# Kernel tuning notes

Hardware: AMD Instinct MI355X
Metric: run time of the kernel (lower is better)

The kernel has to match this reference:

```python
import jax, jax.numpy as jnp
import numpy as np

N, E, G = 40000, 640000, 64
D, H, O = 128, 128, 10
EPS = 1e-5


def _lin(k, fan_in, shape):
    b = 1.0 / np.sqrt(fan_in)
    return jax.random.uniform(k, shape, jnp.float32, -b, b)


def setup_inputs() -> dict:
    key = jax.random.key(0)
    ks = jax.random.split(key, 12)
    x = jax.random.normal(ks[0], (N, D), jnp.float32)
    edge_index = jax.random.randint(ks[1], (2, E), 0, N)
    batch = jnp.sort(jax.random.randint(ks[2], (N,), 0, G))
    return {
        "x": x,
        "edge_index": edge_index,
        "batch": batch,
        "num_graphs": G,
        "W_gcn": _lin(ks[3], D, (D, H)),
        "b_gcn": jnp.zeros((H,), jnp.float32),
        "gamma": jnp.ones((H,), jnp.float32),
        "beta": jnp.zeros((H,), jnp.float32),
        "W1": _lin(ks[4], 3 * H, (3 * H, H)),
        "b1": _lin(ks[5], 3 * H, (H,)),
        "W2": _lin(ks[6], H, (H, H // 2)),
        "b2": _lin(ks[7], H, (H // 2,)),
        "W3": _lin(ks[8], H // 2, (H // 2, O)),
        "b3": _lin(ks[9], H // 2, (O,)),
    }


def reference(x, edge_index, batch, num_graphs, W_gcn, b_gcn, gamma, beta, W1, b1, W2, b2, W3, b3):
    n = x.shape[0]
    src, dst = edge_index[0], edge_index[1]
    # GCNConv: h = D^{-1/2} (A + I) D^{-1/2} (x W) + b  (self-loops, symmetric norm)
    h = x @ W_gcn                                   # [N, H]
    deg = jax.ops.segment_sum(jnp.ones((src.shape[0],), h.dtype), dst, num_segments=n) + 1.0
    dinv = jax.lax.rsqrt(deg)                       # [N]
    coef = dinv[src] * dinv[dst]                    # [E]
    msg = h[src] * coef[:, None]                    # [E, H] gather (memory bound)
    agg = jax.ops.segment_sum(msg, dst, num_segments=n)
    agg = agg + h * (dinv * dinv)[:, None] + b_gcn  # self-loop term + bias
    h = jax.nn.relu(agg)
    # LayerNorm over feature dim
    mu = jnp.mean(h, axis=-1, keepdims=True)
    var = jnp.mean(jnp.square(h - mu), axis=-1, keepdims=True)
    h = (h - mu) * jax.lax.rsqrt(var + EPS) * gamma + beta
    # global mean / add / max pools keyed by graph id
    counts = jax.ops.segment_sum(jnp.ones((n,), h.dtype), batch, num_segments=num_graphs)
    x_add = jax.ops.segment_sum(h, batch, num_segments=num_graphs)
    x_mean = x_add / jnp.maximum(counts, 1.0)[:, None]
    x_max = jax.ops.segment_max(h, batch, num_segments=num_graphs)
    x_max = jnp.where(counts[:, None] > 0, x_max, 0.0)
    g = jnp.concatenate([x_mean, x_add, x_max], axis=1)  # [G, 3H]
    # MLP head (dropout is identity at inference)
    g = jax.nn.relu(g @ W1 + b1)
    g = jax.nn.relu(g @ W2 + b2)
    return g @ W3 + b3
```

## Files before the change

### kernel.cpp

```cpp
#include <hip/hip_runtime.h>
#include <math.h>

#define EPS 1e-5f
#define FLT_BIG 3.402823466e38f

typedef __attribute__((ext_vector_type(8))) short bf16x8;
typedef __attribute__((ext_vector_type(4))) float f32x4;

__device__ __forceinline__ unsigned fflip(float f){
  int i = __float_as_int(f);
  return (unsigned)(i ^ ((i>>31) | 0x80000000));
}
__device__ __forceinline__ float funflip(unsigned u){
  int i = (u & 0x80000000u) ? (int)(u ^ 0x80000000u) : (int)(~u);
  return __int_as_float(i);
}
__device__ __forceinline__ unsigned f2bf(float f){
  unsigned u = __float_as_uint(f);
  return (u + 0x7FFFu + ((u>>16)&1u)) >> 16;
}
__device__ __forceinline__ float bf_lo(unsigned v){ return __uint_as_float(v<<16); }
__device__ __forceinline__ float bf_hi(unsigned v){ return __uint_as_float(v & 0xFFFF0000u); }

__device__ __forceinline__ int lbound(const int* __restrict__ a, int n, int key){
  int lo=0, hi=n;
  while(lo<hi){ int mid=(lo+hi)>>1; if(a[mid]<key) lo=mid+1; else hi=mid; }
  return lo;
}

__global__ __launch_bounds__(256) void k_init(
    int* __restrict__ cursor, int N,
    unsigned* __restrict__ psum, unsigned* __restrict__ pmaxu, int GP,
    const float* __restrict__ Wg, ushort* __restrict__ Wp){
  int i = blockIdx.x*blockDim.x + threadIdx.x;
  if(i<N) cursor[i] = 0;
  if(i<GP){ psum[i]=0u; pmaxu[i]=0u; }
  if(i<2048){
    int tile = i>>6, l = i&63;
    int kt = tile>>3, ct = tile&7;
    int q = l>>4, nn = l&15;
    ushort w8[8];
    #pragma unroll
    for(int j=0;j<8;j++)
      w8[j] = (ushort)f2bf(Wg[(kt*32 + q*8 + j)*128 + ct*16 + nn]);
    ushort* dst = Wp + (size_t)i*8;
    #pragma unroll
    for(int j=0;j<8;j++) dst[j] = w8[j];
  }
}

__global__ void k_scatter(const int* __restrict__ src, const int* __restrict__ dst, int E,
                          int* __restrict__ cursor, int* __restrict__ csr){
  int i = blockIdx.x*blockDim.x + threadIdx.x;
  int e = i<<2;
  if((E&3)==0){
    if(e<E){
      int4 s4 = *(const int4*)(src+e);
      int4 d4 = *(const int4*)(dst+e);
      int p;
      p = atomicAdd(&cursor[d4.x],1); if(p<64) csr[(d4.x<<6)+p] = s4.x;
      p = atomicAdd(&cursor[d4.y],1); if(p<64) csr[(d4.y<<6)+p] = s4.y;
      p = atomicAdd(&cursor[d4.z],1); if(p<64) csr[(d4.z<<6)+p] = s4.z;
      p = atomicAdd(&cursor[d4.w],1); if(p<64) csr[(d4.w<<6)+p] = s4.w;
    }
  } else {
    #pragma unroll
    for(int j=0;j<4;j++){
      int ee = e+j;
      if(ee<E){
        int s = src[ee], d = dst[ee];
        int p = atomicAdd(&cursor[d],1);
        if(p<64) csr[(d<<6)+p] = s;
      }
    }
  }
}

__global__ __launch_bounds__(256) void k_scale(
    const float4* __restrict__ x4, int nq, const int* __restrict__ cursor,
    uint2* __restrict__ xs2){
  int i = blockIdx.x*blockDim.x + threadIdx.x;
  if(i>=nq) return;
  int node = i>>5;
  int deg = cursor[node]; if(deg>64) deg=64;
  float dinv = rsqrtf((float)deg + 1.0f);
  float4 v = x4[i];
  uint2 o;
  o.x = (f2bf(v.y*dinv)<<16) | f2bf(v.x*dinv);
  o.y = (f2bf(v.w*dinv)<<16) | f2bf(v.z*dinv);
  xs2[i] = o;
}

__global__ void k_agg(const uint4* __restrict__ xs4, const int* __restrict__ cursor,
                      const int* __restrict__ csr, int n, uint4* __restrict__ zb4){
  int w = (blockIdx.x*blockDim.x + threadIdx.x)>>6;
  if(w>=n) return;
  int lane = threadIdx.x & 63;
  int grp = lane>>4, li = lane&15;
  int deg = cursor[w]; if(deg>64) deg=64;
  int k0 = w<<6, k1 = k0+deg;
  float dd = rsqrtf((float)deg + 1.0f);
  float a0=0.f,a1=0.f,a2=0.f,a3=0.f,a4=0.f,a5=0.f,a6=0.f,a7=0.f;
  if(grp==0){
    uint4 sv = xs4[(w<<4)+li];
    a0=bf_lo(sv.x); a1=bf_hi(sv.x); a2=bf_lo(sv.y); a3=bf_hi(sv.y);
    a4=bf_lo(sv.z); a5=bf_hi(sv.z); a6=bf_lo(sv.w); a7=bf_hi(sv.w);
  }
  for(int kb=k0; kb<k1; kb+=16){
    int base = kb + (grp<<2);
    int4 s4 = *(const int4*)(csr + base);
    if(base   < k1){ uint4 v = xs4[(s4.x<<4)+li];
      a0+=bf_lo(v.x); a1+=bf_hi(v.x); a2+=bf_lo(v.y); a3+=bf_hi(v.y);
      a4+=bf_lo(v.z); a5+=bf_hi(v.z); a6+=bf_lo(v.w); a7+=bf_hi(v.w); }
    if(base+1 < k1){ uint4 v = xs4[(s4.y<<4)+li];
      a0+=bf_lo(v.x); a1+=bf_hi(v.x); a2+=bf_lo(v.y); a3+=bf_hi(v.y);
      a4+=bf_lo(v.z); a5+=bf_hi(v.z); a6+=bf_lo(v.w); a7+=bf_hi(v.w); }
    if(base+2 < k1){ uint4 v = xs4[(s4.z<<4)+li];
      a0+=bf_lo(v.x); a1+=bf_hi(v.x); a2+=bf_lo(v.y); a3+=bf_hi(v.y);
      a4+=bf_lo(v.z); a5+=bf_hi(v.z); a6+=bf_lo(v.w); a7+=bf_hi(v.w); }
    if(base+3 < k1){ uint4 v = xs4[(s4.w<<4)+li];
      a0+=bf_lo(v.x); a1+=bf_hi(v.x); a2+=bf_lo(v.y); a3+=bf_hi(v.y);
      a4+=bf_lo(v.z); a5+=bf_hi(v.z); a6+=bf_lo(v.w); a7+=bf_hi(v.w); }
  }
  a0 += __shfl_xor(a0,16,64); a1 += __shfl_xor(a1,16,64);
  a2 += __shfl_xor(a2,16,64); a3 += __shfl_xor(a3,16,64);
  a4 += __shfl_xor(a4,16,64); a5 += __shfl_xor(a5,16,64);
  a6 += __shfl_xor(a6,16,64); a7 += __shfl_xor(a7,16,64);
  a0 += __shfl_xor(a0,32,64); a1 += __shfl_xor(a1,32,64);
  a2 += __shfl_xor(a2,32,64); a3 += __shfl_xor(a3,32,64);
  a4 += __shfl_xor(a4,32,64); a5 += __shfl_xor(a5,32,64);
  a6 += __shfl_xor(a6,32,64); a7 += __shfl_xor(a7,32,64);
  if(grp==0){
    uint4 o;
    o.x = (f2bf(a1*dd)<<16) | f2bf(a0*dd);
    o.y = (f2bf(a3*dd)<<16) | f2bf(a2*dd);
    o.z = (f2bf(a5*dd)<<16) | f2bf(a4*dd);
    o.w = (f2bf(a7*dd)<<16) | f2bf(a6*dd);
    zb4[(w<<4)+li] = o;
  }
}

__global__ __launch_bounds__(256) void k_gemmln(
    const unsigned* __restrict__ zb, const ushort* __restrict__ Wp,
    const float* __restrict__ bgc, const float* __restrict__ gamma, const float* __restrict__ beta,
    const int* __restrict__ batch, int n,
    float* __restrict__ pool_sum, unsigned* __restrict__ pool_maxu){
  __shared__ unsigned ztu[64*68];
  int t = threadIdx.x, lane = t & 63, wv = t >> 6;
  int rowBase = blockIdx.x*64;
  {
    int row = t>>2, qo = (t&3)*16;
    unsigned* lp = ztu + row*68 + qo;
    if(rowBase+row < n){
      const uint4* gp = (const uint4*)(zb + (size_t)(rowBase+row)*64 + qo);
      #pragma unroll
      for(int i=0;i<4;i++) ((uint4*)lp)[i] = gp[i];
    }else{
      #pragma unroll
      for(int i=0;i<4;i++) ((uint4*)lp)[i] = make_uint4(0,0,0,0);
    }
  }
  __syncthreads();

  int q = lane>>4, nn = lane&15;
  int m = wv*16 + nn;
  bf16x8 afr[4];
  #pragma unroll
  for(int kt=0;kt<4;kt++)
    afr[kt] = *(const bf16x8*)((const char*)ztu + m*272 + kt*64 + q*16);

  f32x4 acc[8];
  #pragma unroll
  for(int ct=0;ct<8;ct++){
    f32x4 c = {0.f,0.f,0.f,0.f};
    #pragma unroll
    for(int kt=0;kt<4;kt++){
      bf16x8 bfr = *(const bf16x8*)(Wp + ((size_t)(kt*8+ct)*64 + lane)*8);
      c = __builtin_amdgcn_mfma_f32_16x16x32_bf16(afr[kt], bfr, c, 0, 0, 0);
    }
    acc[ct] = c;
  }
  float s[4]={0,0,0,0}, qq[4]={0,0,0,0};
  #pragma unroll
  for(int ct=0;ct<8;ct++){
    float bb = bgc[ct*16+nn];
    #pragma unroll
    for(int r=0;r<4;r++){
      float v = acc[ct][r] + bb;
      v = fmaxf(v, 0.f);
      acc[ct][r] = v;
      s[r] += v; qq[r] += v*v;
    }
  }
  #pragma unroll
  for(int d=1; d<16; d<<=1){
    #pragma unroll
    for(int r=0;r<4;r++){
      s[r]  += __shfl_xor(s[r],  d, 64);
      qq[r] += __shfl_xor(qq[r], d, 64);
    }
  }
  float mu[4], isd[4];
  #pragma unroll
  for(int r=0;r<4;r++){
    mu[r] = s[r]*(1.f/128.f);
    float var = qq[r]*(1.f/128.f) - mu[r]*mu[r];
    isd[r] = rsqrtf(var + EPS);
  }
  #pragma unroll
  for(int ct=0;ct<8;ct++){
    float gm = gamma[ct*16+nn], bt = beta[ct*16+nn];
    #pragma unroll
    for(int r=0;r<4;r++)
      acc[ct][r] = (acc[ct][r]-mu[r])*isd[r]*gm + bt;
  }
  int gbr[4];
  #pragma unroll
  for(int r=0;r<4;r++){
    int gr = rowBase + wv*16 + q*4 + r;
    gbr[r] = (gr < n) ? batch[gr] : -1;
  }
  int b0i = rowBase + wv*16; if(b0i >= n) b0i = n-1;
  int b15i = rowBase + wv*16 + 15; if(b15i >= n) b15i = n-1;
  int gmin = batch[b0i], gmax = batch[b15i];
  if(gmax < gmin) gmax = gmin;
  for(int g=gmin; g<=gmax; ++g){
    #pragma unroll
    for(int ct=0;ct<8;ct++){
      float ssum = 0.f, smax = -FLT_BIG;
      #pragma unroll
      for(int r=0;r<4;r++){
        if(gbr[r]==g){
          ssum += acc[ct][r];
          smax = fmaxf(smax, acc[ct][r]);
        }
      }
      ssum += __shfl_xor(ssum, 16, 64);
      ssum += __shfl_xor(ssum, 32, 64);
      float o1 = __shfl_xor(smax, 16, 64); smax = fmaxf(smax, o1);
      float o2 = __shfl_xor(smax, 32, 64); smax = fmaxf(smax, o2);
      if(q==0){
        if(ssum != 0.f)   atomicAdd(&pool_sum[g*128 + ct*16 + nn], ssum);
        if(smax > -FLT_BIG) atomicMax(&pool_maxu[g*128 + ct*16 + nn], fflip(smax));
      }
    }
  }
}

__global__ void k_head(const float* __restrict__ pool_sum, const unsigned* __restrict__ pool_maxu,
                       const int* __restrict__ batch, int n,
                       const float* __restrict__ W1, const float* __restrict__ b1,
                       const float* __restrict__ W2, const float* __restrict__ b2,
                       const float* __restrict__ W3, const float* __restrict__ b3,
                       float* __restrict__ out){
  int g = blockIdx.x, t = threadIdx.x;
  __shared__ float red[2][128];
  __shared__ float gl[384];
  __shared__ float h1[128];
  __shared__ float h2[64];
  __shared__ int cnt_s;
  if(t==0){
    int s = lbound(batch,n,g), e = lbound(batch,n,g+1);
    cnt_s = e - s;
  }
  __syncthreads();
  int cnt = cnt_s;
  if(t<128){
    float s = pool_sum[g*128+t];
    gl[128+t] = s;
    gl[t] = s / (float)((cnt>1)?cnt:1);
    float m = funflip(pool_maxu[g*128+t]);
    gl[256+t] = (cnt>0) ? m : 0.f;
  }
  __syncthreads();
  int j = t & 127, kh = t >> 7;
  float p=0.f;
  for(int k=kh*192; k<kh*192+192; k++) p += gl[k]*W1[k*128+j];
  red[kh][j]=p;
  __syncthreads();
  if(t<128){
    float v = red[0][t]+red[1][t]+b1[t];
    h1[t]=fmaxf(v,0.f);
  }
  __syncthreads();
  if(t<64){
    float a=b2[t];
    for(int k=0;k<128;k++) a += h1[k]*W2[k*64+t];
    h2[t]=fmaxf(a,0.f);
  }
  __syncthreads();
  if(t<10){
    float a=b3[t];
    for(int k=0;k<64;k++) a += h2[k]*W3[k*10+t];
    out[g*10+t]=a;
  }
}

extern "C" void kernel_launch(void* const* d_in, const int* in_sizes, int n_in,
                              void* d_out, int out_size, void* d_ws, size_t ws_size,
                              hipStream_t stream){
  const float* x     = (const float*)d_in[0];
  const int*   ei    = (const int*)d_in[1];
  const int*   batch = (const int*)d_in[2];
  const float* Wg    = (const float*)d_in[4];
  const float* bg    = (const float*)d_in[5];
  const float* gamma = (const float*)d_in[6];
  const float* beta  = (const float*)d_in[7];
  const float* W1    = (const float*)d_in[8];
  const float* b1    = (const float*)d_in[9];
  const float* W2    = (const float*)d_in[10];
  const float* b2    = (const float*)d_in[11];
  const float* W3    = (const float*)d_in[12];
  const float* b3    = (const float*)d_in[13];
  float* out = (float*)d_out;

  int N = in_sizes[0]/128;
  int E = in_sizes[1]/2;
  const int G = 64;
  const int* src = ei;
  const int* dst = ei + E;

  char* p = (char*)d_ws;
  auto alloc=[&](size_t bytes)->char*{ char* r=p; p += (bytes+255)&~(size_t)255; return r; };
  int*      cursor = (int*)     alloc((size_t)N*4);
  int*      csr    = (int*)     alloc((size_t)N*64*4);
  unsigned* zb     = (unsigned*)alloc((size_t)N*64*4);
  float*    psum   = (float*)   alloc((size_t)G*128*4);
  unsigned* pmaxu  = (unsigned*)alloc((size_t)G*128*4);
  unsigned* xs     = (unsigned*)alloc((size_t)N*64*4);
  ushort*   Wp     = (ushort*)  alloc(2048*8*2);

  int GP = G*128;
  int nq = N*32;
  int ib = (N+255)/256;
  k_init<<<ib,256,0,stream>>>(cursor,N,(unsigned*)psum,pmaxu,GP,Wg,Wp);
  int eb = (E/4 + 255)/256;
  k_scatter<<<eb,256,0,stream>>>(src,dst,E,cursor,csr);
  int sb = (nq+255)/256;
  k_scale<<<sb,256,0,stream>>>((const float4*)x,nq,cursor,(uint2*)xs);
  int ab = (int)(((size_t)N*64 + 255)/256);
  k_agg<<<ab,256,0,stream>>>((const uint4*)xs,cursor,csr,N,(uint4*)zb);
  k_gemmln<<<(N+63)/64,256,0,stream>>>(zb,Wp,bg,gamma,beta,batch,N,psum,pmaxu);
  k_head<<<G,256,0,stream>>>(psum,pmaxu,batch,N,W1,b1,W2,b2,W3,b3,out);
}
```

Baseline: 180.9 us.

## Fuse neighbor aggregation with GEMM/LayerNorm/pooling and precompute graph counts

```diff
diff --git a/kernel.cpp b/kernel.cpp
--- a/kernel.cpp
+++ b/kernel.cpp
@@ -31,10 +31,15 @@
 __global__ __launch_bounds__(256) void k_init(
     int* __restrict__ cursor, int N,
     unsigned* __restrict__ psum, unsigned* __restrict__ pmaxu, int GP,
-    const float* __restrict__ Wg, ushort* __restrict__ Wp){
+    const float* __restrict__ Wg, ushort* __restrict__ Wp,
+    const int* __restrict__ batch, int* __restrict__ gcnt, int G){
   int i = blockIdx.x*blockDim.x + threadIdx.x;
   if(i<N) cursor[i] = 0;
   if(i<GP){ psum[i]=0u; pmaxu[i]=0u; }
+  if(i<G){
+    int s = lbound(batch,N,i), e = lbound(batch,N,i+1);
+    gcnt[i] = e - s;
+  }
   if(i<2048){
     int tile = i>>6, l = i&63;
     int kt = tile>>3, ct = tile&7;
@@ -91,83 +96,74 @@
   xs2[i] = o;
 }
 
-__global__ void k_agg(const uint4* __restrict__ xs4, const int* __restrict__ cursor,
-                      const int* __restrict__ csr, int n, uint4* __restrict__ zb4){
-  int w = (blockIdx.x*blockDim.x + threadIdx.x)>>6;
-  if(w>=n) return;
-  int lane = threadIdx.x & 63;
+__global__ __launch_bounds__(256) void k_aggemm(
+    const uint4* __restrict__ xs4, const int* __restrict__ cursor,
+    const int* __restrict__ csr, int n,
+    const ushort* __restrict__ Wp,
+    const float* __restrict__ bgc, const float* __restrict__ gamma, const float* __restrict__ beta,
+    const int* __restrict__ batch,
+    float* __restrict__ pool_sum, unsigned* __restrict__ pool_maxu){
+  __shared__ unsigned ztu[16*68];
+  int t = threadIdx.x, lane = t & 63, wv = t >> 6;
   int grp = lane>>4, li = lane&15;
-  int deg = cursor[w]; if(deg>64) deg=64;
-  int k0 = w<<6, k1 = k0+deg;
-  float dd = rsqrtf((float)deg + 1.0f);
-  float a0=0.f,a1=0.f,a2=0.f,a3=0.f,a4=0.f,a5=0.f,a6=0.f,a7=0.f;
-  if(grp==0){
-    uint4 sv = xs4[(w<<4)+li];
-    a0=bf_lo(sv.x); a1=bf_hi(sv.x); a2=bf_lo(sv.y); a3=bf_hi(sv.y);
-    a4=bf_lo(sv.z); a5=bf_hi(sv.z); a6=bf_lo(sv.w); a7=bf_hi(sv.w);
-  }
-  for(int kb=k0; kb<k1; kb+=16){
-    int base = kb + (grp<<2);
-    int4 s4 = *(const int4*)(csr + base);
-    if(base   < k1){ uint4 v = xs4[(s4.x<<4)+li];
-      a0+=bf_lo(v.x); a1+=bf_hi(v.x); a2+=bf_lo(v.y); a3+=bf_hi(v.y);
-      a4+=bf_lo(v.z); a5+=bf_hi(v.z); a6+=bf_lo(v.w); a7+=bf_hi(v.w); }
-    if(base+1 < k1){ uint4 v = xs4[(s4.y<<4)+li];
-      a0+=bf_lo(v.x); a1+=bf_hi(v.x); a2+=bf_lo(v.y); a3+=bf_hi(v.y);
-      a4+=bf_lo(v.z); a5+=bf_hi(v.z); a6+=bf_lo(v.w); a7+=bf_hi(v.w); }
-    if(base+2 < k1){ uint4 v = xs4[(s4.z<<4)+li];
-      a0+=bf_lo(v.x); a1+=bf_hi(v.x); a2+=bf_lo(v.y); a3+=bf_hi(v.y);
-      a4+=bf_lo(v.z); a5+=bf_hi(v.z); a6+=bf_lo(v.w); a7+=bf_hi(v.w); }
-    if(base+3 < k1){ uint4 v = xs4[(s4.w<<4)+li];
-      a0+=bf_lo(v.x); a1+=bf_hi(v.x); a2+=bf_lo(v.y); a3+=bf_hi(v.y);
-      a4+=bf_lo(v.z); a5+=bf_hi(v.z); a6+=bf_lo(v.w); a7+=bf_hi(v.w); }
-  }
-  a0 += __shfl_xor(a0,16,64); a1 += __shfl_xor(a1,16,64);
-  a2 += __shfl_xor(a2,16,64); a3 += __shfl_xor(a3,16,64);
-  a4 += __shfl_xor(a4,16,64); a5 += __shfl_xor(a5,16,64);
-  a6 += __shfl_xor(a6,16,64); a7 += __shfl_xor(a7,16,64);
-  a0 += __shfl_xor(a0,32,64); a1 += __shfl_xor(a1,32,64);
-  a2 += __shfl_xor(a2,32,64); a3 += __shfl_xor(a3,32,64);
-  a4 += __shfl_xor(a4,32,64); a5 += __shfl_xor(a5,32,64);
-  a6 += __shfl_xor(a6,32,64); a7 += __shfl_xor(a7,32,64);
-  if(grp==0){
-    uint4 o;
-    o.x = (f2bf(a1*dd)<<16) | f2bf(a0*dd);
-    o.y = (f2bf(a3*dd)<<16) | f2bf(a2*dd);
-    o.z = (f2bf(a5*dd)<<16) | f2bf(a4*dd);
-    o.w = (f2bf(a7*dd)<<16) | f2bf(a6*dd);
-    zb4[(w<<4)+li] = o;
-  }
-}
-
-__global__ __launch_bounds__(256) void k_gemmln(
-    const unsigned* __restrict__ zb, const ushort* __restrict__ Wp,
-    const float* __restrict__ bgc, const float* __restrict__ gamma, const float* __restrict__ beta,
-    const int* __restrict__ batch, int n,
-    float* __restrict__ pool_sum, unsigned* __restrict__ pool_maxu){
-  __shared__ unsigned ztu[64*68];
-  int t = threadIdx.x, lane = t & 63, wv = t >> 6;
-  int rowBase = blockIdx.x*64;
-  {
-    int row = t>>2, qo = (t&3)*16;
-    unsigned* lp = ztu + row*68 + qo;
-    if(rowBase+row < n){
-      const uint4* gp = (const uint4*)(zb + (size_t)(rowBase+row)*64 + qo);
-      #pragma unroll
-      for(int i=0;i<4;i++) ((uint4*)lp)[i] = gp[i];
-    }else{
-      #pragma unroll
-      for(int i=0;i<4;i++) ((uint4*)lp)[i] = make_uint4(0,0,0,0);
-    }
-  }
-  __syncthreads();
+  int rowBase = blockIdx.x*16;
+
+  for(int j=0;j<4;j++){
+    int rl = wv*4 + j;
+    int node = rowBase + rl;
+    float a0=0.f,a1=0.f,a2=0.f,a3=0.f,a4=0.f,a5=0.f,a6=0.f,a7=0.f;
+    float dd = 1.f;
+    if(node < n){
+      int deg = cursor[node]; if(deg>64) deg=64;
+      dd = rsqrtf((float)deg + 1.0f);
+      int k0 = node<<6, k1 = k0+deg;
+      if(grp==0){
+        uint4 sv = xs4[(node<<4)+li];
+        a0=bf_lo(sv.x); a1=bf_hi(sv.x); a2=bf_lo(sv.y); a3=bf_hi(sv.y);
+        a4=bf_lo(sv.z); a5=bf_hi(sv.z); a6=bf_lo(sv.w); a7=bf_hi(sv.w);
+      }
+      for(int kb=k0; kb<k1; kb+=16){
+        int base = kb + (grp<<2);
+        int4 s4 = *(const int4*)(csr + base);
+        if(base   < k1){ uint4 v = xs4[(s4.x<<4)+li];
+          a0+=bf_lo(v.x); a1+=bf_hi(v.x); a2+=bf_lo(v.y); a3+=bf_hi(v.y);
+          a4+=bf_lo(v.z); a5+=bf_hi(v.z); a6+=bf_lo(v.w); a7+=bf_hi(v.w); }
+        if(base+1 < k1){ uint4 v = xs4[(s4.y<<4)+li];
+          a0+=bf_lo(v.x); a1+=bf_hi(v.x); a2+=bf_lo(v.y); a3+=bf_hi(v.y);
+          a4+=bf_lo(v.z); a5+=bf_hi(v.z); a6+=bf_lo(v.w); a7+=bf_hi(v.w); }
+        if(base+2 < k1){ uint4 v = xs4[(s4.z<<4)+li];
+          a0+=bf_lo(v.x); a1+=bf_hi(v.x); a2+=bf_lo(v.y); a3+=bf_hi(v.y);
+          a4+=bf_lo(v.z); a5+=bf_hi(v.z); a6+=bf_lo(v.w); a7+=bf_hi(v.w); }
+        if(base+3 < k1){ uint4 v = xs4[(s4.w<<4)+li];
+          a0+=bf_lo(v.x); a1+=bf_hi(v.x); a2+=bf_lo(v.y); a3+=bf_hi(v.y);
+          a4+=bf_lo(v.z); a5+=bf_hi(v.z); a6+=bf_lo(v.w); a7+=bf_hi(v.w); }
+      }
+    }
+    a0 += __shfl_xor(a0,16,64); a1 += __shfl_xor(a1,16,64);
+    a2 += __shfl_xor(a2,16,64); a3 += __shfl_xor(a3,16,64);
+    a4 += __shfl_xor(a4,16,64); a5 += __shfl_xor(a5,16,64);
+    a6 += __shfl_xor(a6,16,64); a7 += __shfl_xor(a7,16,64);
+    a0 += __shfl_xor(a0,32,64); a1 += __shfl_xor(a1,32,64);
+    a2 += __shfl_xor(a2,32,64); a3 += __shfl_xor(a3,32,64);
+    a4 += __shfl_xor(a4,32,64); a5 += __shfl_xor(a5,32,64);
+    a6 += __shfl_xor(a6,32,64); a7 += __shfl_xor(a7,32,64);
+    if(grp==0){
+      uint4 o;
+      o.x = (f2bf(a1*dd)<<16) | f2bf(a0*dd);
+      o.y = (f2bf(a3*dd)<<16) | f2bf(a2*dd);
+      o.z = (f2bf(a5*dd)<<16) | f2bf(a4*dd);
+      o.w = (f2bf(a7*dd)<<16) | f2bf(a6*dd);
+      ((uint4*)(ztu + rl*68))[li] = o;
+    }
+  }
+  __syncthreads();
+  if(wv != 0) return;
 
   int q = lane>>4, nn = lane&15;
-  int m = wv*16 + nn;
   bf16x8 afr[4];
   #pragma unroll
   for(int kt=0;kt<4;kt++)
-    afr[kt] = *(const bf16x8*)((const char*)ztu + m*272 + kt*64 + q*16);
+    afr[kt] = *(const bf16x8*)((const char*)ztu + nn*272 + kt*64 + q*16);
 
   f32x4 acc[8];
   #pragma unroll
@@ -217,11 +213,11 @@
   int gbr[4];
   #pragma unroll
   for(int r=0;r<4;r++){
-    int gr = rowBase + wv*16 + q*4 + r;
+    int gr = rowBase + q*4 + r;
     gbr[r] = (gr < n) ? batch[gr] : -1;
   }
-  int b0i = rowBase + wv*16; if(b0i >= n) b0i = n-1;
-  int b15i = rowBase + wv*16 + 15; if(b15i >= n) b15i = n-1;
+  int b0i = rowBase; if(b0i >= n) b0i = n-1;
+  int b15i = rowBase + 15; if(b15i >= n) b15i = n-1;
   int gmin = batch[b0i], gmax = batch[b15i];
   if(gmax < gmin) gmax = gmin;
   for(int g=gmin; g<=gmax; ++g){
@@ -240,7 +236,7 @@
       float o1 = __shfl_xor(smax, 16, 64); smax = fmaxf(smax, o1);
       float o2 = __shfl_xor(smax, 32, 64); smax = fmaxf(smax, o2);
       if(q==0){
-        if(ssum != 0.f)   atomicAdd(&pool_sum[g*128 + ct*16 + nn], ssum);
+        if(ssum != 0.f)     atomicAdd(&pool_sum[g*128 + ct*16 + nn], ssum);
         if(smax > -FLT_BIG) atomicMax(&pool_maxu[g*128 + ct*16 + nn], fflip(smax));
       }
     }
@@ -248,7 +244,7 @@
 }
 
 __global__ void k_head(const float* __restrict__ pool_sum, const unsigned* __restrict__ pool_maxu,
-                       const int* __restrict__ batch, int n,
+                       const int* __restrict__ gcnt,
                        const float* __restrict__ W1, const float* __restrict__ b1,
                        const float* __restrict__ W2, const float* __restrict__ b2,
                        const float* __restrict__ W3, const float* __restrict__ b3,
@@ -258,13 +254,7 @@
   __shared__ float gl[384];
   __shared__ float h1[128];
   __shared__ float h2[64];
-  __shared__ int cnt_s;
-  if(t==0){
-    int s = lbound(batch,n,g), e = lbound(batch,n,g+1);
-    cnt_s = e - s;
-  }
-  __syncthreads();
-  int cnt = cnt_s;
+  int cnt = gcnt[g];
   if(t<128){
     float s = pool_sum[g*128+t];
     gl[128+t] = s;
@@ -324,22 +314,21 @@
   auto alloc=[&](size_t bytes)->char*{ char* r=p; p += (bytes+255)&~(size_t)255; return r; };
   int*      cursor = (int*)     alloc((size_t)N*4);
   int*      csr    = (int*)     alloc((size_t)N*64*4);
-  unsigned* zb     = (unsigned*)alloc((size_t)N*64*4);
   float*    psum   = (float*)   alloc((size_t)G*128*4);
   unsigned* pmaxu  = (unsigned*)alloc((size_t)G*128*4);
   unsigned* xs     = (unsigned*)alloc((size_t)N*64*4);
   ushort*   Wp     = (ushort*)  alloc(2048*8*2);
+  int*      gcnt   = (int*)     alloc((size_t)G*4);
 
   int GP = G*128;
   int nq = N*32;
   int ib = (N+255)/256;
-  k_init<<<ib,256,0,stream>>>(cursor,N,(unsigned*)psum,pmaxu,GP,Wg,Wp);
+  k_init<<<ib,256,0,stream>>>(cursor,N,(unsigned*)psum,pmaxu,GP,Wg,Wp,batch,gcnt,G);
   int eb = (E/4 + 255)/256;
   k_scatter<<<eb,256,0,stream>>>(src,dst,E,cursor,csr);
   int sb = (nq+255)/256;
   k_scale<<<sb,256,0,stream>>>((const float4*)x,nq,cursor,(uint2*)xs);
-  int ab = (int)(((size_t)N*64 + 255)/256);
-  k_agg<<<ab,256,0,stream>>>((const uint4*)xs,cursor,csr,N,(uint4*)zb);
-  k_gemmln<<<(N+63)/64,256,0,stream>>>(zb,Wp,bg,gamma,beta,batch,N,psum,pmaxu);
-  k_head<<<G,256,0,stream>>>(psum,pmaxu,batch,N,W1,b1,W2,b2,W3,b3,out);
-}
+  int nb = (N+15)/16;
+  k_aggemm<<<nb,256,0,stream>>>((const uint4*)xs,cursor,csr,N,Wp,bg,gamma,beta,batch,psum,pmaxu);
+  k_head<<<G,256,0,stream>>>(psum,pmaxu,gcnt,W1,b1,W2,b2,W3,b3,out);
+}
```

Measured after the change: 207.1 us. 14.4% more time.
